# Kernel optimization log

Measured on AMD Instinct MI355X. Metric: run time of the kernel, lower is better.

## Reference

```python
import jax, jax.numpy as jnp
import numpy as np

N, E, F_IN, F_OUT, PERIODS = 40000, 640000, 64, 128, 12


def setup_inputs() -> dict:
    key = jax.random.key(0)
    ks = jax.random.split(key, 24)
    def w(k, shape):
        return jax.random.normal(k, shape, jnp.float32) * 0.05
    inp = {
        "X": jax.random.normal(ks[0], (N, F_IN, PERIODS), jnp.float32),
        "edge_index": jax.random.randint(ks[1], (2, E), 0, N),
        "edge_weight": jax.random.uniform(ks[2], (E,), jnp.float32),
        "attention": jax.random.uniform(ks[3], (PERIODS,), jnp.float32),
    }
    for idx, g in enumerate(["i", "f", "c", "o"]):
        inp[f"W_x{g}"] = w(ks[4 + 4 * idx], (F_IN, F_OUT))
        inp[f"b_x{g}"] = jnp.zeros((F_OUT,), jnp.float32)
        inp[f"W_h{g}"] = w(ks[5 + 4 * idx], (2 * F_OUT, F_OUT))
        inp[f"b_h{g}"] = jnp.zeros((F_OUT,), jnp.float32)
    return inp


def reference(X, edge_index, edge_weight, attention,
              W_xi, b_xi, W_hi, b_hi,
              W_xf, b_xf, W_hf, b_hf,
              W_xc, b_xc, W_hc, b_hc,
              W_xo, b_xo, W_ho, b_ho):
    n = X.shape[0]
    # GCN normalization with self-loops: D^-1/2 (A + I) D^-1/2
    loops = jnp.arange(n)
    rows = jnp.concatenate([edge_index[0], loops])  # sources
    cols = jnp.concatenate([edge_index[1], loops])  # targets
    wts = jnp.concatenate([edge_weight, jnp.ones((n,), X.dtype)])
    deg = jax.ops.segment_sum(wts, cols, num_segments=n)
    dinv = jnp.where(deg > 0, jax.lax.rsqrt(deg), 0.0)
    norm = dinv[rows] * wts * dinv[cols]  # [E+N]

    def gcn(x, W, b):
        xw = x @ W  # [N, F_OUT]
        agg = jax.ops.segment_sum(norm[:, None] * xw[rows], cols, num_segments=n)
        return agg + b

    probs = jax.nn.softmax(attention)
    H0 = jnp.zeros((n, W_hi.shape[1]), X.dtype)
    C0 = jnp.zeros_like(H0)
    Xp = jnp.moveaxis(X, 2, 0)  # [periods, N, F_IN]

    def step(carry, xs):
        H, C, Hacc = carry
        x_t, p = xs
        def gate(Wx, bx, Wh, bh):
            return jnp.concatenate([gcn(x_t, Wx, bx), H], axis=1) @ Wh + bh
        I = jax.nn.sigmoid(gate(W_xi, b_xi, W_hi, b_hi))
        F = jax.nn.sigmoid(gate(W_xf, b_xf, W_hf, b_hf))
        Ct = jnp.tanh(gate(W_xc, b_xc, W_hc, b_hc))
        O = jax.nn.sigmoid(gate(W_xo, b_xo, W_ho, b_ho))
        C_new = F * C + I * Ct
        H_new = O * jnp.tanh(C_new)
        return (H_new, C_new, Hacc + p * H_new), None

    (H, C, Hacc), _ = jax.lax.scan(step, (H0, C0, H0), (Xp, probs))
    return Hacc
```

## Files before the change

### kernel.cpp

```cpp
#include <hip/hip_runtime.h>

typedef __bf16 bf16_t;
typedef bf16_t bf16x4 __attribute__((ext_vector_type(4)));
typedef bf16_t bf16x8 __attribute__((ext_vector_type(8)));
typedef float floatx4 __attribute__((ext_vector_type(4)));

#define F_INq 64
#define F_OUTq 128
#define PERIODSq 12
#define XROW (F_INq * PERIODSq)

__global__ __launch_bounds__(256) void k_init(float* deg, int* counts, int N) {
  int i = blockIdx.x * 256 + threadIdx.x;
  if (i < N) { deg[i] = 1.0f; counts[i] = 0; }
}

__global__ __launch_bounds__(256) void k_accum(const int* __restrict__ ei, const float* __restrict__ ew,
                                               float* deg, int* counts, int E) {
  int e = blockIdx.x * 256 + threadIdx.x;
  if (e < E) {
    int c = ei[E + e];
    atomicAdd(&deg[c], ew[e]);
    atomicAdd(&counts[c], 1);
  }
}

__global__ __launch_bounds__(256) void k_dinv(float* deg, int N) {
  int i = blockIdx.x * 256 + threadIdx.x;
  if (i < N) { float d = deg[i]; deg[i] = d > 0.0f ? rsqrtf(d) : 0.0f; }
}

__global__ __launch_bounds__(256) void k_scanA(const int* __restrict__ counts, int* __restrict__ bsum, int N) {
  __shared__ int ws[4];
  int b = blockIdx.x, t = threadIdx.x;
  int base = b * 1024 + t * 4;
  int s = 0;
  if (base + 3 < N) {
    int4 c = *(const int4*)(counts + base);
    s = c.x + c.y + c.z + c.w;
  } else {
    for (int k = 0; k < 4; ++k) if (base + k < N) s += counts[base + k];
  }
  for (int off = 1; off < 64; off <<= 1) s += __shfl_xor(s, off);
  int lane = t & 63, w = t >> 6;
  if (lane == 0) ws[w] = s;
  __syncthreads();
  if (t == 0) bsum[b] = ws[0] + ws[1] + ws[2] + ws[3];
}

__global__ __launch_bounds__(64) void k_scanB(const int* __restrict__ bsum, int* __restrict__ bbase, int nb) {
  int t = threadIdx.x;
  int v = t < nb ? bsum[t] : 0;
  int inc = v;
  for (int off = 1; off < 64; off <<= 1) {
    int u = __shfl_up(inc, off);
    if (t >= off) inc += u;
  }
  if (t < nb) bbase[t] = inc - v;
  if (t == nb - 1) bbase[nb] = inc;
}

__global__ __launch_bounds__(256) void k_scanC(const int* __restrict__ counts, const int* __restrict__ bbase,
                                               int* __restrict__ offs, int* __restrict__ cursor, int N, int nb) {
  __shared__ int ws[4];
  int b = blockIdx.x, t = threadIdx.x;
  int base = b * 1024 + t * 4;
  int c0_ = 0, c1_ = 0, c2_ = 0, c3_ = 0;
  if (base + 3 < N) {
    int4 c = *(const int4*)(counts + base);
    c0_ = c.x; c1_ = c.y; c2_ = c.z; c3_ = c.w;
  } else {
    if (base < N) c0_ = counts[base];
    if (base + 1 < N) c1_ = counts[base + 1];
    if (base + 2 < N) c2_ = counts[base + 2];
    if (base + 3 < N) c3_ = counts[base + 3];
  }
  int tot = c0_ + c1_ + c2_ + c3_;
  int lane = t & 63, w = t >> 6;
  int inc = tot;
  for (int off = 1; off < 64; off <<= 1) {
    int u = __shfl_up(inc, off);
    if (lane >= off) inc += u;
  }
  if (lane == 63) ws[w] = inc;
  __syncthreads();
  int wb = bbase[b];
  for (int i = 0; i < w; ++i) wb += ws[i];
  int e = wb + inc - tot;
  if (base < N)     { offs[base] = e;                 cursor[base] = e; }
  if (base + 1 < N) { int o = e + c0_;                offs[base + 1] = o; cursor[base + 1] = o; }
  if (base + 2 < N) { int o = e + c0_ + c1_;          offs[base + 2] = o; cursor[base + 2] = o; }
  if (base + 3 < N) { int o = e + c0_ + c1_ + c2_;    offs[base + 3] = o; cursor[base + 3] = o; }
  if (b == 0 && t == 0) offs[N] = bbase[nb];
}

__global__ __launch_bounds__(1024) void k_scan(const int* __restrict__ counts, int* __restrict__ offs,
                                               int* __restrict__ cursor, int N) {
  __shared__ int sd[1024];
  int t = threadIdx.x;
  int CH = (N + 1023) >> 10;
  int base = t * CH;
  int sum = 0;
  for (int i = 0; i < CH; ++i) { int idx = base + i; if (idx < N) sum += counts[idx]; }
  sd[t] = sum;
  __syncthreads();
  for (int off = 1; off < 1024; off <<= 1) {
    int v = (t >= off) ? sd[t - off] : 0;
    __syncthreads();
    sd[t] += v;
    __syncthreads();
  }
  int run = sd[t] - sum;
  for (int i = 0; i < CH; ++i) {
    int idx = base + i;
    if (idx < N) { offs[idx] = run; cursor[idx] = run; run += counts[idx]; }
  }
  if (t == 1023) offs[N] = sd[1023];
}

__global__ __launch_bounds__(256) void k_scatter(const int* __restrict__ ei, const float* __restrict__ ew,
                                                 const float* __restrict__ dinv, int* cursor,
                                                 int* __restrict__ csr_src, float* __restrict__ csr_nrm, int E) {
  int e = blockIdx.x * 256 + threadIdx.x;
  if (e < E) {
    int r = ei[e], c = ei[E + e];
    int p = atomicAdd(&cursor[c], 1);
    csr_src[p] = r;
    csr_nrm[p] = dinv[r] * ew[e] * dinv[c];
  }
}

__global__ __launch_bounds__(256) void k_prew(
    const float* __restrict__ Wxi, const float* __restrict__ Whi,
    const float* __restrict__ Wxf, const float* __restrict__ Whf,
    const float* __restrict__ Wxc, const float* __restrict__ Whc,
    const float* __restrict__ Wxo, const float* __restrict__ Who,
    const float* __restrict__ bxi, const float* __restrict__ bhi,
    const float* __restrict__ bxf, const float* __restrict__ bhf,
    const float* __restrict__ bxc, const float* __restrict__ bhc,
    const float* __restrict__ bxo, const float* __restrict__ bho,
    const float* __restrict__ att,
    bf16_t* __restrict__ WbT, float* __restrict__ bcomb, float* __restrict__ probs) {
  const int WT = 512 * 192;
  int gid = blockIdx.x * 256 + threadIdx.x;
  if (gid < WT) {
    int col = gid / 192, k = gid % 192;
    int g = col >> 7, j = col & 127;
    const float* Wx = g == 0 ? Wxi : g == 1 ? Wxf : g == 2 ? Wxc : Wxo;
    const float* Wh = g == 0 ? Whi : g == 1 ? Whf : g == 2 ? Whc : Who;
    float s;
    if (k < 64) {
      s = 0.0f;
      for (int kk = 0; kk < 128; ++kk) s += Wx[k * 128 + kk] * Wh[kk * 128 + j];
    } else {
      s = Wh[(k + 64) * 128 + j];
    }
    WbT[(size_t)col * 192 + k] = (bf16_t)s;
  } else if (gid < WT + 512) {
    int cc = gid - WT;
    int g = cc >> 7, j = cc & 127;
    const float* bx = g == 0 ? bxi : g == 1 ? bxf : g == 2 ? bxc : bxo;
    const float* bh = g == 0 ? bhi : g == 1 ? bhf : g == 2 ? bhc : bho;
    const float* Wh = g == 0 ? Whi : g == 1 ? Whf : g == 2 ? Whc : Who;
    float s = bh[j];
    for (int kk = 0; kk < 128; ++kk) s += bx[kk] * Wh[kk * 128 + j];
    bcomb[cc] = s;
  } else if (gid == WT + 512) {
    float m = att[0];
    for (int i = 1; i < PERIODSq; ++i) m = fmaxf(m, att[i]);
    float e[PERIODSq], s = 0.0f;
    for (int i = 0; i < PERIODSq; ++i) { e[i] = __expf(att[i] - m); s += e[i]; }
    for (int i = 0; i < PERIODSq; ++i) probs[i] = e[i] / s;
  }
}

__global__ __launch_bounds__(192) void k_xpose(const float* __restrict__ X, bf16_t* __restrict__ Xb) {
  __shared__ float lds[XROW];
  const int n = blockIdx.x, tid = threadIdx.x;
  const float4* Xr = (const float4*)(X + (size_t)n * XROW);
  float4 v = Xr[tid];
  lds[tid * 4 + 0] = v.x;
  lds[tid * 4 + 1] = v.y;
  lds[tid * 4 + 2] = v.z;
  lds[tid * 4 + 3] = v.w;
  __syncthreads();
  const int o = tid * 4;
  bf16x4 r;
#pragma unroll
  for (int k = 0; k < 4; ++k) {
    int oo = o + k;
    int tt = oo >> 6, f = oo & 63;
    r[k] = (bf16_t)lds[f * PERIODSq + tt];
  }
  *(bf16x4*)(Xb + (size_t)n * XROW + o) = r;
}

__global__ __launch_bounds__(256) void k_agg2(const bf16_t* __restrict__ Xb, const int* __restrict__ csr_src,
                                              const float* __restrict__ csr_nrm, const int* __restrict__ offs,
                                              const float* __restrict__ dinv, bf16_t* __restrict__ Xagg, int N) {
  const int node = blockIdx.x * 4 + (threadIdx.x >> 6);
  const int lane = threadIdx.x & 63;
  const int s0 = offs[node], s1 = offs[node + 1];
  floatx4 a0 = {0.f, 0.f, 0.f, 0.f}, a1 = a0, a2 = a0;
  int e = s0;
  for (; e + 8 <= s1; e += 8) {
    bf16x4 v[8][3];
    float nn[8];
#pragma unroll
    for (int u = 0; u < 8; ++u) {
      int s = csr_src[e + u];
      nn[u] = csr_nrm[e + u];
      const bf16x4* xp = (const bf16x4*)(Xb + (size_t)s * XROW) + lane;
      v[u][0] = xp[0]; v[u][1] = xp[64]; v[u][2] = xp[128];
    }
#pragma unroll
    for (int u = 0; u < 8; ++u) {
#pragma unroll
      for (int k = 0; k < 4; ++k) {
        a0[k] += nn[u] * (float)v[u][0][k];
        a1[k] += nn[u] * (float)v[u][1][k];
        a2[k] += nn[u] * (float)v[u][2][k];
      }
    }
  }
  for (; e < s1; ++e) {
    int s = csr_src[e];
    float nr = csr_nrm[e];
    const bf16x4* xp = (const bf16x4*)(Xb + (size_t)s * XROW) + lane;
    bf16x4 v0 = xp[0], v1 = xp[64], v2 = xp[128];
#pragma unroll
    for (int k = 0; k < 4; ++k) {
      a0[k] += nr * (float)v0[k];
      a1[k] += nr * (float)v1[k];
      a2[k] += nr * (float)v2[k];
    }
  }
  float dc = dinv[node];
  float self = dc * dc;
  const bf16x4* xc = (const bf16x4*)(Xb + (size_t)node * XROW) + lane;
  {
    bf16x4 v0 = xc[0], v1 = xc[64], v2 = xc[128];
#pragma unroll
    for (int k = 0; k < 4; ++k) {
      a0[k] += self * (float)v0[k];
      a1[k] += self * (float)v1[k];
      a2[k] += self * (float)v2[k];
    }
  }
  const int f4 = lane & 15, tq = lane >> 4;
  floatx4 accs[3] = {a0, a1, a2};
#pragma unroll
  for (int j = 0; j < 3; ++j) {
    int tt = tq + 4 * j;
    bf16x4 r;
#pragma unroll
    for (int k = 0; k < 4; ++k) r[k] = (bf16_t)accs[j][k];
    *(bf16x4*)(Xagg + ((size_t)tt * N + node) * 64 + f4 * 4) = r;
  }
}

__global__ __launch_bounds__(256) void k_agg(const float* __restrict__ X, const int* __restrict__ csr_src,
                                             const float* __restrict__ csr_nrm, const int* __restrict__ offs,
                                             const float* __restrict__ dinv, bf16_t* __restrict__ Xagg, int N) {
  int c = blockIdx.x;
  int tid = threadIdx.x;
  int s0 = offs[c], s1 = offs[c + 1];
  const int i0 = tid, i1 = tid + 256, i2 = tid + 512;
  float a0 = 0.f, a1 = 0.f, a2 = 0.f;
  for (int e = s0; e < s1; ++e) {
    int s = csr_src[e];
    float nr = csr_nrm[e];
    const float* xp = X + (size_t)s * XROW;
    a0 += nr * xp[i0]; a1 += nr * xp[i1]; a2 += nr * xp[i2];
  }
  float dc = dinv[c];
  float self = dc * dc;
  const float* xc = X + (size_t)c * XROW;
  a0 += self * xc[i0]; a1 += self * xc[i1]; a2 += self * xc[i2];
  __shared__ float lds[XROW];
  lds[i0] = a0; lds[i1] = a1; lds[i2] = a2;
  __syncthreads();
  for (int o = tid; o < XROW; o += 256) {
    int tt = o >> 6, f = o & 63;
    Xagg[(size_t)tt * N * 64 + (size_t)c * 64 + f] = (bf16_t)lds[f * PERIODSq + tt];
  }
}

__global__ __launch_bounds__(512, 2) void k_gate_all(const bf16_t* __restrict__ Xagg,
                                                     const bf16_t* __restrict__ WbT,
                                                     const float* __restrict__ bcomb,
                                                     const float* __restrict__ probs,
                                                     float* __restrict__ out, int N) {
  __shared__ __align__(16) char Hs[2][32 * 256];
  const int tid = threadIdx.x;
  const int lane = tid & 63, w = tid >> 6;
  const int q = lane >> 4, c0 = lane & 15;
  const int n0 = blockIdx.x * 32;
  const int swz = c0 & 7;

  bf16x8 Wf[4][6];
#pragma unroll
  for (int g = 0; g < 4; ++g) {
    const bf16_t* wp = WbT + (size_t)((g * 8 + w) * 16 + c0) * 192;
#pragma unroll
    for (int ks = 0; ks < 6; ++ks) Wf[g][ks] = *(const bf16x8*)(wp + ks * 32 + q * 8);
  }
  floatx4 bv[4];
#pragma unroll
  for (int g = 0; g < 4; ++g) bv[g] = *(const floatx4*)(bcomb + g * 128 + w * 16 + q * 4);

  floatx4 Cst[2], Ha[2];
#pragma unroll
  for (int rt = 0; rt < 2; ++rt) {
    Cst[rt] = (floatx4){0.f, 0.f, 0.f, 0.f};
    Ha[rt] = (floatx4){0.f, 0.f, 0.f, 0.f};
  }

  const bf16_t* Xrow0 = Xagg + (size_t)(n0 + c0) * 64 + q * 8;
  const bf16_t* Xrow1 = Xagg + (size_t)(n0 + 16 + c0) * 64 + q * 8;

  bf16x8 Xf0 = *(const bf16x8*)(Xrow0);
  bf16x8 Xf1 = *(const bf16x8*)(Xrow0 + 32);
  bf16x8 Xf2 = *(const bf16x8*)(Xrow1);
  bf16x8 Xf3 = *(const bf16x8*)(Xrow1 + 32);

  floatx4 accA[2][4], accB[2][4];
#pragma unroll
  for (int g = 0; g < 4; ++g) { accA[0][g] = bv[g]; accA[1][g] = bv[g]; }
#pragma unroll
  for (int g = 0; g < 4; ++g) {
    accA[0][g] = __builtin_amdgcn_mfma_f32_16x16x32_bf16(Wf[g][0], Xf0, accA[0][g], 0, 0, 0);
    accA[0][g] = __builtin_amdgcn_mfma_f32_16x16x32_bf16(Wf[g][1], Xf1, accA[0][g], 0, 0, 0);
    accA[1][g] = __builtin_amdgcn_mfma_f32_16x16x32_bf16(Wf[g][0], Xf2, accA[1][g], 0, 0, 0);
    accA[1][g] = __builtin_amdgcn_mfma_f32_16x16x32_bf16(Wf[g][1], Xf3, accA[1][g], 0, 0, 0);
  }

  const float NL2E = -1.44269504f;
  const float T2L2E = 2.88539008f;

#define PERIOD(T, AC, AN, RB, WB, DO_H, DO_NEXT)                                                      \
  do {                                                                                                \
    if (DO_NEXT) {                                                                                    \
      const size_t toff_ = (size_t)((T) + 1) * N * 64;                                                \
      Xf0 = *(const bf16x8*)(Xrow0 + toff_);                                                          \
      Xf1 = *(const bf16x8*)(Xrow0 + toff_ + 32);                                                     \
      Xf2 = *(const bf16x8*)(Xrow1 + toff_);                                                          \
      Xf3 = *(const bf16x8*)(Xrow1 + toff_ + 32);                                                     \
    }                                                                                                 \
    if (DO_H) {                                                                                       \
      _Pragma("unroll") for (int ks = 0; ks < 4; ++ks) {                                              \
        bf16x8 B0 = *(const bf16x8*)(&Hs[RB][(c0) * 256 + (((4 * ks + q) ^ swz) << 4)]);              \
        bf16x8 B1 = *(const bf16x8*)(&Hs[RB][(16 + c0) * 256 + (((4 * ks + q) ^ swz) << 4)]);         \
        _Pragma("unroll") for (int g = 0; g < 4; ++g) {                                               \
          AC[0][g] = __builtin_amdgcn_mfma_f32_16x16x32_bf16(Wf[g][ks + 2], B0, AC[0][g], 0, 0, 0);   \
          AC[1][g] = __builtin_amdgcn_mfma_f32_16x16x32_bf16(Wf[g][ks + 2], B1, AC[1][g], 0, 0, 0);   \
        }                                                                                             \
      }                                                                                               \
    }                                                                                                 \
    const float pt_ = probs[T];                                                                       \
    _Pragma("unroll") for (int rt = 0; rt < 2; ++rt) {                                                \
      bf16x4 hv_;                                                                                     \
      _Pragma("unroll") for (int r = 0; r < 4; ++r) {                                                 \
        float pI = AC[rt][0][r], pF = AC[rt][1][r], pC = AC[rt][2][r], pO = AC[rt][3][r];             \
        float I_ = __builtin_amdgcn_rcpf(1.0f + __builtin_amdgcn_exp2f(pI * NL2E));                   \
        float F_ = __builtin_amdgcn_rcpf(1.0f + __builtin_amdgcn_exp2f(pF * NL2E));                   \
        float Ct_ = fmaf(-2.0f, __builtin_amdgcn_rcpf(1.0f + __builtin_amdgcn_exp2f(pC * T2L2E)), 1.0f); \
        float O_ = __builtin_amdgcn_rcpf(1.0f + __builtin_amdgcn_exp2f(pO * NL2E));                   \
        float Cn_ = fmaf(F_, Cst[rt][r], I_ * Ct_);                                                   \
        Cst[rt][r] = Cn_;                                                                             \
        float tC_ = fmaf(-2.0f, __builtin_amdgcn_rcpf(1.0f + __builtin_amdgcn_exp2f(Cn_ * T2L2E)), 1.0f); \
        float Hn_ = O_ * tC_;                                                                         \
        Ha[rt][r] = fmaf(pt_, Hn_, Ha[rt][r]);                                                        \
        hv_[r] = (bf16_t)Hn_;                                                                         \
      }                                                                                               \
      *(bf16x4*)(&Hs[WB][(rt * 16 + c0) * 256 + (((2 * w + (q >> 1)) ^ swz) << 4) + ((q & 1) * 8)]) = hv_; \
    }                                                                                                 \
    if (DO_NEXT) {                                                                                    \
      _Pragma("unroll") for (int g = 0; g < 4; ++g) { AN[0][g] = bv[g]; AN[1][g] = bv[g]; }           \
      _Pragma("unroll") for (int g = 0; g < 4; ++g) {                                                 \
        AN[0][g] = __builtin_amdgcn_mfma_f32_16x16x32_bf16(Wf[g][0], Xf0, AN[0][g], 0, 0, 0);         \
        AN[0][g] = __builtin_amdgcn_mfma_f32_16x16x32_bf16(Wf[g][1], Xf1, AN[0][g], 0, 0, 0);         \
        AN[1][g] = __builtin_amdgcn_mfma_f32_16x16x32_bf16(Wf[g][0], Xf2, AN[1][g], 0, 0, 0);         \
        AN[1][g] = __builtin_amdgcn_mfma_f32_16x16x32_bf16(Wf[g][1], Xf3, AN[1][g], 0, 0, 0);         \
      }                                                                                               \
    }                                                                                                 \
    __syncthreads();                                                                                  \
  } while (0)

  PERIOD(0, accA, accB, 1, 0, 0, 1);
  for (int tt = 1; tt <= 9; tt += 2) {
    PERIOD(tt, accB, accA, 0, 1, 1, 1);
    PERIOD(tt + 1, accA, accB, 1, 0, 1, 1);
  }
  PERIOD(11, accB, accA, 0, 1, 1, 0);
#undef PERIOD

#pragma unroll
  for (int rt = 0; rt < 2; ++rt) {
    int row = n0 + rt * 16 + c0;
    *(floatx4*)(out + (size_t)row * 128 + w * 16 + q * 4) = Ha[rt];
  }
}

extern "C" void kernel_launch(void* const* d_in, const int* in_sizes, int n_in,
                              void* d_out, int out_size, void* d_ws, size_t ws_size,
                              hipStream_t stream) {
  const float* X = (const float*)d_in[0];
  const int* ei = (const int*)d_in[1];
  const float* ew = (const float*)d_in[2];
  const float* att = (const float*)d_in[3];
  const float* Wxi = (const float*)d_in[4];
  const float* bxi = (const float*)d_in[5];
  const float* Whi = (const float*)d_in[6];
  const float* bhi = (const float*)d_in[7];
  const float* Wxf = (const float*)d_in[8];
  const float* bxf = (const float*)d_in[9];
  const float* Whf = (const float*)d_in[10];
  const float* bhf = (const float*)d_in[11];
  const float* Wxc = (const float*)d_in[12];
  const float* bxc = (const float*)d_in[13];
  const float* Whc = (const float*)d_in[14];
  const float* bhc = (const float*)d_in[15];
  const float* Wxo = (const float*)d_in[16];
  const float* bxo = (const float*)d_in[17];
  const float* Who = (const float*)d_in[18];
  const float* bho = (const float*)d_in[19];
  float* out = (float*)d_out;

  const int N = in_sizes[0] / XROW;
  const int E = in_sizes[2];

  char* base = (char*)d_ws;
  size_t off = 0;
  auto carve = [&](size_t bytes) {
    char* r = base + off;
    off += (bytes + 255) & ~(size_t)255;
    return (void*)r;
  };
  float* deg = (float*)carve((size_t)N * 4);
  int* counts = (int*)carve((size_t)N * 4);
  int* offs = (int*)carve((size_t)(N + 1) * 4);
  int* cursor = (int*)carve((size_t)(N + 1) * 4);
  int* csr_src = (int*)carve((size_t)E * 4);
  float* csr_nrm = (float*)carve((size_t)E * 4);
  bf16_t* WbT = (bf16_t*)carve((size_t)512 * 192 * 2);
  float* bcomb = (float*)carve(512 * 4);
  float* probs = (float*)carve(64);
  int* bsum = (int*)carve(64 * 4);
  int* bbase = (int*)carve(68 * 4);
  bf16_t* Xagg = (bf16_t*)carve((size_t)PERIODSq * N * 64 * 2);
  bf16_t* Xb = (bf16_t*)carve((size_t)N * XROW * 2);
  const bool use_bf16 = (off <= ws_size);

  k_init<<<(N + 255) / 256, 256, 0, stream>>>(deg, counts, N);
  k_accum<<<(E + 255) / 256, 256, 0, stream>>>(ei, ew, deg, counts, E);
  k_dinv<<<(N + 255) / 256, 256, 0, stream>>>(deg, N);
  const int nb = (N + 1023) >> 10;
  if (nb <= 64) {
    k_scanA<<<nb, 256, 0, stream>>>(counts, bsum, N);
    k_scanB<<<1, 64, 0, stream>>>(bsum, bbase, nb);
    k_scanC<<<nb, 256, 0, stream>>>(counts, bbase, offs, cursor, N, nb);
  } else {
    k_scan<<<1, 1024, 0, stream>>>(counts, offs, cursor, N);
  }
  k_scatter<<<(E + 255) / 256, 256, 0, stream>>>(ei, ew, deg, cursor, csr_src, csr_nrm, E);
  k_prew<<<(512 * 192 + 512 + 1 + 255) / 256, 256, 0, stream>>>(
      Wxi, Whi, Wxf, Whf, Wxc, Whc, Wxo, Who,
      bxi, bhi, bxf, bhf, bxc, bhc, bxo, bho, att, WbT, bcomb, probs);

  if (use_bf16) {
    k_xpose<<<N, 192, 0, stream>>>(X, Xb);
    k_agg2<<<N / 4, 256, 0, stream>>>(Xb, csr_src, csr_nrm, offs, deg, Xagg, N);
  } else {
    k_agg<<<N, 256, 0, stream>>>(X, csr_src, csr_nrm, offs, deg, Xagg, N);
  }

  k_gate_all<<<N / 32, 512, 0, stream>>>(Xagg, WbT, bcomb, probs, out, N);
}
```

Measured before the change: 604.5 us.

## Split aggregation per period, fuse dinv into scan, drop scanB, preload probs

Replaces the per-node aggregation kernel with one that launches a block per (period, node-group). Each wave processes four edges at a time, with lanes split into edge groups and a shuffle reduction. This raises parallelism and cache locality per period, at the cost of re-reading edge lists twelve times. Also folds the dinv computation into scanA and removes scanB by having each scanC block sum the preceding block totals, which cuts kernel launches. In the gate kernel it preloads attention probs into registers and feeds the bias directly as the MFMA accumulator input.

```diff
diff --git a/kernel.cpp b/kernel.cpp
--- a/kernel.cpp
+++ b/kernel.cpp
@@ -30,7 +30,8 @@
   if (i < N) { float d = deg[i]; deg[i] = d > 0.0f ? rsqrtf(d) : 0.0f; }
 }
 
-__global__ __launch_bounds__(256) void k_scanA(const int* __restrict__ counts, int* __restrict__ bsum, int N) {
+__global__ __launch_bounds__(256) void k_scanA(const int* __restrict__ counts, float* __restrict__ deg,
+                                               int* __restrict__ bsum, int N) {
   __shared__ int ws[4];
   int b = blockIdx.x, t = threadIdx.x;
   int base = b * 1024 + t * 4;
@@ -41,6 +42,11 @@
   } else {
     for (int k = 0; k < 4; ++k) if (base + k < N) s += counts[base + k];
   }
+#pragma unroll
+  for (int k = 0; k < 4; ++k) {
+    int idx = base + k;
+    if (idx < N) { float d = deg[idx]; deg[idx] = d > 0.0f ? rsqrtf(d) : 0.0f; }
+  }
   for (int off = 1; off < 64; off <<= 1) s += __shfl_xor(s, off);
   int lane = t & 63, w = t >> 6;
   if (lane == 0) ws[w] = s;
@@ -48,19 +54,7 @@
   if (t == 0) bsum[b] = ws[0] + ws[1] + ws[2] + ws[3];
 }
 
-__global__ __launch_bounds__(64) void k_scanB(const int* __restrict__ bsum, int* __restrict__ bbase, int nb) {
-  int t = threadIdx.x;
-  int v = t < nb ? bsum[t] : 0;
-  int inc = v;
-  for (int off = 1; off < 64; off <<= 1) {
-    int u = __shfl_up(inc, off);
-    if (t >= off) inc += u;
-  }
-  if (t < nb) bbase[t] = inc - v;
-  if (t == nb - 1) bbase[nb] = inc;
-}
-
-__global__ __launch_bounds__(256) void k_scanC(const int* __restrict__ counts, const int* __restrict__ bbase,
+__global__ __launch_bounds__(256) void k_scanC(const int* __restrict__ counts, const int* __restrict__ bsum,
                                                int* __restrict__ offs, int* __restrict__ cursor, int N, int nb) {
   __shared__ int ws[4];
   int b = blockIdx.x, t = threadIdx.x;
@@ -84,14 +78,19 @@
   }
   if (lane == 63) ws[w] = inc;
   __syncthreads();
-  int wb = bbase[b];
+  int wb = 0;
+  for (int i = 0; i < b; ++i) wb += bsum[i];
   for (int i = 0; i < w; ++i) wb += ws[i];
   int e = wb + inc - tot;
   if (base < N)     { offs[base] = e;                 cursor[base] = e; }
   if (base + 1 < N) { int o = e + c0_;                offs[base + 1] = o; cursor[base + 1] = o; }
   if (base + 2 < N) { int o = e + c0_ + c1_;          offs[base + 2] = o; cursor[base + 2] = o; }
   if (base + 3 < N) { int o = e + c0_ + c1_ + c2_;    offs[base + 3] = o; cursor[base + 3] = o; }
-  if (b == 0 && t == 0) offs[N] = bbase[nb];
+  if (b == nb - 1 && t == 0) {
+    int tt2 = 0;
+    for (int i = 0; i < nb - 1; ++i) tt2 += bsum[i];
+    offs[N] = tt2 + ws[0] + ws[1] + ws[2] + ws[3];
+  }
 }
 
 __global__ __launch_bounds__(1024) void k_scan(const int* __restrict__ counts, int* __restrict__ offs,
@@ -195,67 +194,39 @@
   *(bf16x4*)(Xb + (size_t)n * XROW + o) = r;
 }
 
-__global__ __launch_bounds__(256) void k_agg2(const bf16_t* __restrict__ Xb, const int* __restrict__ csr_src,
+__global__ __launch_bounds__(256) void k_agg3(const bf16_t* __restrict__ Xb, const int* __restrict__ csr_src,
                                               const float* __restrict__ csr_nrm, const int* __restrict__ offs,
                                               const float* __restrict__ dinv, bf16_t* __restrict__ Xagg, int N) {
-  const int node = blockIdx.x * 4 + (threadIdx.x >> 6);
+  const int nbpp = N >> 2;
+  const int t = blockIdx.x / nbpp;
+  const int node = (blockIdx.x % nbpp) * 4 + (threadIdx.x >> 6);
   const int lane = threadIdx.x & 63;
+  const int eg = lane >> 4, fo = lane & 15;
   const int s0 = offs[node], s1 = offs[node + 1];
-  floatx4 a0 = {0.f, 0.f, 0.f, 0.f}, a1 = a0, a2 = a0;
-  int e = s0;
-  for (; e + 8 <= s1; e += 8) {
-    bf16x4 v[8][3];
-    float nn[8];
-#pragma unroll
-    for (int u = 0; u < 8; ++u) {
-      int s = csr_src[e + u];
-      nn[u] = csr_nrm[e + u];
-      const bf16x4* xp = (const bf16x4*)(Xb + (size_t)s * XROW) + lane;
-      v[u][0] = xp[0]; v[u][1] = xp[64]; v[u][2] = xp[128];
-    }
-#pragma unroll
-    for (int u = 0; u < 8; ++u) {
-#pragma unroll
-      for (int k = 0; k < 4; ++k) {
-        a0[k] += nn[u] * (float)v[u][0][k];
-        a1[k] += nn[u] * (float)v[u][1][k];
-        a2[k] += nn[u] * (float)v[u][2][k];
-      }
-    }
-  }
-  for (; e < s1; ++e) {
-    int s = csr_src[e];
-    float nr = csr_nrm[e];
-    const bf16x4* xp = (const bf16x4*)(Xb + (size_t)s * XROW) + lane;
-    bf16x4 v0 = xp[0], v1 = xp[64], v2 = xp[128];
-#pragma unroll
-    for (int k = 0; k < 4; ++k) {
-      a0[k] += nr * (float)v0[k];
-      a1[k] += nr * (float)v1[k];
-      a2[k] += nr * (float)v2[k];
-    }
-  }
-  float dc = dinv[node];
-  float self = dc * dc;
-  const bf16x4* xc = (const bf16x4*)(Xb + (size_t)node * XROW) + lane;
-  {
-    bf16x4 v0 = xc[0], v1 = xc[64], v2 = xc[128];
-#pragma unroll
-    for (int k = 0; k < 4; ++k) {
-      a0[k] += self * (float)v0[k];
-      a1[k] += self * (float)v1[k];
-      a2[k] += self * (float)v2[k];
-    }
-  }
-  const int f4 = lane & 15, tq = lane >> 4;
-  floatx4 accs[3] = {a0, a1, a2};
-#pragma unroll
-  for (int j = 0; j < 3; ++j) {
-    int tt = tq + 4 * j;
+  floatx4 a = {0.f, 0.f, 0.f, 0.f};
+  for (int e = s0; e < s1; e += 4) {
+    int idx = e + eg;
+    bool v = idx < s1;
+    int ce = v ? idx : s1 - 1;
+    float nr = v ? csr_nrm[ce] : 0.0f;
+    int src = csr_src[ce];
+    bf16x4 x = *(const bf16x4*)(Xb + (size_t)src * XROW + t * 64 + fo * 4);
+#pragma unroll
+    for (int k = 0; k < 4; ++k) a[k] += nr * (float)x[k];
+  }
+#pragma unroll
+  for (int k = 0; k < 4; ++k) {
+    a[k] += __shfl_xor(a[k], 16);
+    a[k] += __shfl_xor(a[k], 32);
+  }
+  if (eg == 0) {
+    float dc = dinv[node];
+    float self = dc * dc;
+    bf16x4 xs = *(const bf16x4*)(Xb + (size_t)node * XROW + t * 64 + fo * 4);
     bf16x4 r;
 #pragma unroll
-    for (int k = 0; k < 4; ++k) r[k] = (bf16_t)accs[j][k];
-    *(bf16x4*)(Xagg + ((size_t)tt * N + node) * 64 + f4 * 4) = r;
+    for (int k = 0; k < 4; ++k) r[k] = (bf16_t)(a[k] + self * (float)xs[k]);
+    *(bf16x4*)(Xagg + ((size_t)t * N + node) * 64 + fo * 4) = r;
   }
 }
 
@@ -308,6 +279,9 @@
   floatx4 bv[4];
 #pragma unroll
   for (int g = 0; g < 4; ++g) bv[g] = *(const floatx4*)(bcomb + g * 128 + w * 16 + q * 4);
+  float pr[PERIODSq];
+#pragma unroll
+  for (int i = 0; i < PERIODSq; ++i) pr[i] = probs[i];
 
   floatx4 Cst[2], Ha[2];
 #pragma unroll
@@ -326,12 +300,10 @@
 
   floatx4 accA[2][4], accB[2][4];
 #pragma unroll
-  for (int g = 0; g < 4; ++g) { accA[0][g] = bv[g]; accA[1][g] = bv[g]; }
-#pragma unroll
   for (int g = 0; g < 4; ++g) {
-    accA[0][g] = __builtin_amdgcn_mfma_f32_16x16x32_bf16(Wf[g][0], Xf0, accA[0][g], 0, 0, 0);
+    accA[0][g] = __builtin_amdgcn_mfma_f32_16x16x32_bf16(Wf[g][0], Xf0, bv[g], 0, 0, 0);
     accA[0][g] = __builtin_amdgcn_mfma_f32_16x16x32_bf16(Wf[g][1], Xf1, accA[0][g], 0, 0, 0);
-    accA[1][g] = __builtin_amdgcn_mfma_f32_16x16x32_bf16(Wf[g][0], Xf2, accA[1][g], 0, 0, 0);
+    accA[1][g] = __builtin_amdgcn_mfma_f32_16x16x32_bf16(Wf[g][0], Xf2, bv[g], 0, 0, 0);
     accA[1][g] = __builtin_amdgcn_mfma_f32_16x16x32_bf16(Wf[g][1], Xf3, accA[1][g], 0, 0, 0);
   }
 
@@ -357,7 +329,7 @@
         }                                                                                             \
       }                                                                                               \
     }                                                                                                 \
-    const float pt_ = probs[T];                                                                       \
+    const float pt_ = pr[T];                                                                          \
     _Pragma("unroll") for (int rt = 0; rt < 2; ++rt) {                                                \
       bf16x4 hv_;                                                                                     \
       _Pragma("unroll") for (int r = 0; r < 4; ++r) {                                                 \
@@ -376,11 +348,10 @@
       *(bf16x4*)(&Hs[WB][(rt * 16 + c0) * 256 + (((2 * w + (q >> 1)) ^ swz) << 4) + ((q & 1) * 8)]) = hv_; \
     }                                                                                                 \
     if (DO_NEXT) {                                                                                    \
-      _Pragma("unroll") for (int g = 0; g < 4; ++g) { AN[0][g] = bv[g]; AN[1][g] = bv[g]; }           \
       _Pragma("unroll") for (int g = 0; g < 4; ++g) {                                                 \
-        AN[0][g] = __builtin_amdgcn_mfma_f32_16x16x32_bf16(Wf[g][0], Xf0, AN[0][g], 0, 0, 0);         \
+        AN[0][g] = __builtin_amdgcn_mfma_f32_16x16x32_bf16(Wf[g][0], Xf0, bv[g], 0, 0, 0);            \
         AN[0][g] = __builtin_amdgcn_mfma_f32_16x16x32_bf16(Wf[g][1], Xf1, AN[0][g], 0, 0, 0);         \
-        AN[1][g] = __builtin_amdgcn_mfma_f32_16x16x32_bf16(Wf[g][0], Xf2, AN[1][g], 0, 0, 0);         \
+        AN[1][g] = __builtin_amdgcn_mfma_f32_16x16x32_bf16(Wf[g][0], Xf2, bv[g], 0, 0, 0);            \
         AN[1][g] = __builtin_amdgcn_mfma_f32_16x16x32_bf16(Wf[g][1], Xf3, AN[1][g], 0, 0, 0);         \
       }                                                                                               \
     }                                                                                                 \
@@ -447,20 +418,18 @@
   float* bcomb = (float*)carve(512 * 4);
   float* probs = (float*)carve(64);
   int* bsum = (int*)carve(64 * 4);
-  int* bbase = (int*)carve(68 * 4);
   bf16_t* Xagg = (bf16_t*)carve((size_t)PERIODSq * N * 64 * 2);
   bf16_t* Xb = (bf16_t*)carve((size_t)N * XROW * 2);
   const bool use_bf16 = (off <= ws_size);
 
   k_init<<<(N + 255) / 256, 256, 0, stream>>>(deg, counts, N);
   k_accum<<<(E + 255) / 256, 256, 0, stream>>>(ei, ew, deg, counts, E);
-  k_dinv<<<(N + 255) / 256, 256, 0, stream>>>(deg, N);
   const int nb = (N + 1023) >> 10;
   if (nb <= 64) {
-    k_scanA<<<nb, 256, 0, stream>>>(counts, bsum, N);
-    k_scanB<<<1, 64, 0, stream>>>(bsum, bbase, nb);
-    k_scanC<<<nb, 256, 0, stream>>>(counts, bbase, offs, cursor, N, nb);
+    k_scanA<<<nb, 256, 0, stream>>>(counts, deg, bsum, N);
+    k_scanC<<<nb, 256, 0, stream>>>(counts, bsum, offs, cursor, N, nb);
   } else {
+    k_dinv<<<(N + 255) / 256, 256, 0, stream>>>(deg, N);
     k_scan<<<1, 1024, 0, stream>>>(counts, offs, cursor, N);
   }
   k_scatter<<<(E + 255) / 256, 256, 0, stream>>>(ei, ew, deg, cursor, csr_src, csr_nrm, E);
@@ -468,9 +437,9 @@
       Wxi, Whi, Wxf, Whf, Wxc, Whc, Wxo, Who,
       bxi, bhi, bxf, bhf, bxc, bhc, bxo, bho, att, WbT, bcomb, probs);
 
-  if (use_bf16) {
+  if (use_bf16 && (N & 3) == 0) {
     k_xpose<<<N, 192, 0, stream>>>(X, Xb);
-    k_agg2<<<N / 4, 256, 0, stream>>>(Xb, csr_src, csr_nrm, offs, deg, Xagg, N);
+    k_agg3<<<PERIODSq * (N >> 2), 256, 0, stream>>>(Xb, csr_src, csr_nrm, offs, deg, Xagg, N);
   } else {
     k_agg<<<N, 256, 0, stream>>>(X, csr_src, csr_nrm, offs, deg, Xagg, N);
   }
```

Result: slower. 736.2 us (+21.8%).
